# Optimization experiments

Measured on AMD Instinct MI355X. Metric: run time of the kernel, lower is better.

Reference implementation:

```python
import jax, jax.numpy as jnp
import numpy as np

S, B, H = 256, 64, 1024


def setup_inputs() -> dict:
    key = jax.random.key(0)
    ks = jax.random.split(key, 8)
    scale = 1.0 / np.sqrt(2 * H)  # nn.Linear default-ish scale
    return {
        "x": jax.random.normal(ks[0], (S, B, H), dtype=jnp.float32),
        "h0": jax.random.normal(ks[1], (B, H), dtype=jnp.float32),
        "c0": jax.random.normal(ks[2], (B, H), dtype=jnp.float32),
        "Wf": jax.random.normal(ks[3], (H, 2 * H), dtype=jnp.float32) * scale,
        "bf": jnp.zeros((H,), dtype=jnp.float32),
        "Wi": jax.random.normal(ks[4], (H, 2 * H), dtype=jnp.float32) * scale,
        "bi": jnp.zeros((H,), dtype=jnp.float32),
        "Wg": jax.random.normal(ks[5], (H, 2 * H), dtype=jnp.float32) * scale,
        "bg": jnp.zeros((H,), dtype=jnp.float32),
        "Wo": jax.random.normal(ks[6], (H, 2 * H), dtype=jnp.float32) * scale,
        "bo": jnp.zeros((H,), dtype=jnp.float32),
    }


def _lstm(x, h0, c0, Wf, bf, Wi, bi, Wg, bg, Wo, bo):
    nhid = h0.shape[-1]
    # Fuse the 4 gate Linears into one GEMM: W_all [4H, 2H], b_all [4H].
    W_all = jnp.concatenate([Wf, Wi, Wg, Wo], axis=0)
    b_all = jnp.concatenate([bf, bi, bg, bo], axis=0)
    Wx, Wh = W_all[:, :nhid], W_all[:, nhid:]  # x-part / h-part of cat([x,h])
    # Precompute input contribution for all timesteps: [S, B, 4H]
    xz = jnp.einsum("sbh,gh->sbg", x, Wx) + b_all

    def step(carry, xz_t):
        h, c = carry
        z = xz_t + h @ Wh.T  # [B, 4H]
        f, i, g, o = jnp.split(z, 4, axis=-1)
        f = jax.nn.sigmoid(f)
        i = jax.nn.sigmoid(i)
        g = jnp.tanh(g)
        o = jax.nn.sigmoid(o)
        c = f * c + i * g
        h = o * jnp.tanh(c)
        return (h, c), h

    (h_f, c_f), hseq = jax.lax.scan(step, (h0, c0), xz)
    return hseq, h_f, c_f


def reference(x, h0, c0, Wf, bf, Wi, bi, Wg, bg, Wo, bo):
    hseq, h_f, c_f = _lstm(x, h0, c0, Wf, bf, Wi, bi, Wg, bg, Wo, bo)
    # residual_con=False path in the original: return x + hidden_seq
    return x + hseq, h_f, c_f
```

## Files before the change

kernel.cpp:

```cpp
#include <hip/hip_runtime.h>

typedef __bf16 bf16x8 __attribute__((ext_vector_type(8)));
typedef float f32x4 __attribute__((ext_vector_type(4)));
typedef unsigned int u32x4 __attribute__((ext_vector_type(4)));

#define S_LEN 256
#define BATCH 64
#define HID   1024
#define NWG   256
#define SBH   (S_LEN * BATCH * HID)
#define BH    (BATCH * HID)
#define BAR_INTS 256

__device__ __forceinline__ float sigm(float v) { return 1.0f / (1.0f + __expf(-v)); }
__device__ __forceinline__ float tanh_fast(float v) {
  float e = __expf(-2.0f * __builtin_fabsf(v));
  float r = (1.0f - e) / (1.0f + e);
  return __builtin_copysignf(r, v);
}

__device__ __forceinline__ u32x4 cvt8(float4 a, float4 b) {
  union { unsigned short us[8]; u32x4 v; } r;
  r.us[0] = __builtin_bit_cast(unsigned short, (__bf16)a.x);
  r.us[1] = __builtin_bit_cast(unsigned short, (__bf16)a.y);
  r.us[2] = __builtin_bit_cast(unsigned short, (__bf16)a.z);
  r.us[3] = __builtin_bit_cast(unsigned short, (__bf16)a.w);
  r.us[4] = __builtin_bit_cast(unsigned short, (__bf16)b.x);
  r.us[5] = __builtin_bit_cast(unsigned short, (__bf16)b.y);
  r.us[6] = __builtin_bit_cast(unsigned short, (__bf16)b.z);
  r.us[7] = __builtin_bit_cast(unsigned short, (__bf16)b.w);
  return r.v;
}

#define LOAD8_X4(dst, base, MODS)                                             \
  asm volatile(                                                               \
      "global_load_dwordx4 %0, %8, off offset:0 " MODS "\n\t"                 \
      "global_load_dwordx4 %1, %8, off offset:64 " MODS "\n\t"                \
      "global_load_dwordx4 %2, %8, off offset:128 " MODS "\n\t"               \
      "global_load_dwordx4 %3, %8, off offset:192 " MODS "\n\t"               \
      "global_load_dwordx4 %4, %8, off offset:256 " MODS "\n\t"               \
      "global_load_dwordx4 %5, %8, off offset:320 " MODS "\n\t"               \
      "global_load_dwordx4 %6, %8, off offset:384 " MODS "\n\t"               \
      "global_load_dwordx4 %7, %8, off offset:448 " MODS "\n\t"               \
      "s_waitcnt vmcnt(0)"                                                    \
      : "=&v"((dst)[0]), "=&v"((dst)[1]), "=&v"((dst)[2]), "=&v"((dst)[3]),   \
        "=&v"((dst)[4]), "=&v"((dst)[5]), "=&v"((dst)[6]), "=&v"((dst)[7])    \
      : "v"(base)                                                             \
      : "memory")

__global__ void prep_kernel(const float* __restrict__ x, const float* __restrict__ h0,
                            const float* __restrict__ Wf, const float* __restrict__ Wi,
                            const float* __restrict__ Wg, const float* __restrict__ Wo,
                            __bf16* __restrict__ x_bf, __bf16* __restrict__ w_x,
                            __bf16* __restrict__ w_h, __bf16* __restrict__ h_buf,
                            int* __restrict__ bar) {
  size_t tid = (size_t)blockIdx.x * blockDim.x + threadIdx.x;
  size_t stride = (size_t)gridDim.x * blockDim.x;

  for (size_t i = tid; i < (size_t)(SBH / 8); i += stride) {
    const float4* s = (const float4*)x + i * 2;
    ((u32x4*)x_bf)[i] = cvt8(s[0], s[1]);
  }

#define W_CONV(W, gidx)                                                        \
  for (size_t i = tid; i < (size_t)(1024 * 128); i += stride) {                \
    int j   = (int)(i >> 7);                                                   \
    int kc8 = (int)(i & 127);                                                  \
    const float* row = (W) + (size_t)j * 2048;                                 \
    const float4* sx = (const float4*)(row + kc8 * 8);                         \
    const float4* sh = (const float4*)(row + 1024 + kc8 * 8);                  \
    size_t dst = (size_t)((gidx) * 1024 + j) * 128 + kc8;                      \
    ((u32x4*)w_x)[dst] = cvt8(sx[0], sx[1]);                                   \
    ((u32x4*)w_h)[dst] = cvt8(sh[0], sh[1]);                                   \
  }
  W_CONV(Wf, 0)
  W_CONV(Wi, 1)
  W_CONV(Wg, 2)
  W_CONV(Wo, 3)
#undef W_CONV

  for (size_t i = tid; i < (size_t)(BH / 8); i += stride) {
    const float4* s = (const float4*)h0 + i * 2;
    ((u32x4*)h_buf)[i] = cvt8(s[0], s[1]);
  }

  for (size_t i = tid; i < BAR_INTS; i += stride) bar[i] = 0;
}

__global__ __launch_bounds__(256, 1) void lstm_kernel(
    const float* __restrict__ x, const float* __restrict__ c0,
    const float* __restrict__ bfp, const float* __restrict__ bip,
    const float* __restrict__ bgp, const float* __restrict__ bop,
    const __bf16* __restrict__ x_bf, const __bf16* __restrict__ w_x,
    const __bf16* __restrict__ w_h, __bf16* __restrict__ h_buf,
    int* __restrict__ bar, float* __restrict__ out) {
  const int tid    = threadIdx.x;
  const int wgid   = blockIdx.x;
  const int m_idx  = wgid & 3;
  const int m_base = m_idx * 16;
  const int U      = (wgid >> 2) * 16;
  const int wave   = tid >> 6;
  const int lane   = tid & 63;
  const int l16    = lane & 15;
  const int kq8    = (lane >> 4) * 8;
  const int kbase  = wave * 256;
  const int wg_in_grp = wgid >> 2;

  int* slots = bar + m_idx * 64;

  __shared__ float zbuf[4][16][65];
  __shared__ __bf16 hpack[16][16];

  u32x4 Braw[64];
#pragma unroll
  for (int n = 0; n < 4; ++n) {
    unsigned long gbh =
        (unsigned long)(w_h + (size_t)(n * 1024 + U + l16) * HID + kbase + kq8);
    LOAD8_X4(&Braw[n * 8], gbh, "");
  }
#pragma unroll
  for (int n = 0; n < 4; ++n) {
    unsigned long gbx =
        (unsigned long)(w_x + (size_t)(n * 1024 + U + l16) * HID + kbase + kq8);
    LOAD8_X4(&Braw[32 + n * 8], gbx, "");
  }

  const int b_loc  = tid >> 4;
  const int u_loc  = tid & 15;
  const int j_t    = U + u_loc;
  const int b_glob = m_base + b_loc;
  float c = c0[(size_t)b_glob * HID + j_t];
  const float bias_f = bfp[j_t], bias_i = bip[j_t], bias_g = bgp[j_t], bias_o = bop[j_t];

  u32x4 Araw_x[8];
  {
    const __bf16* xp = x_bf + (size_t)(m_base + l16) * HID + kbase + kq8;
#pragma unroll
    for (int kc = 0; kc < 8; ++kc) Araw_x[kc] = *(const u32x4*)(xp + kc * 32);
  }
  f32x4 accx0 = {0,0,0,0}, accx1 = {0,0,0,0}, accx2 = {0,0,0,0}, accx3 = {0,0,0,0};
#pragma unroll
  for (int kc = 0; kc < 8; ++kc) {
    bf16x8 a = __builtin_bit_cast(bf16x8, Araw_x[kc]);
    accx0 = __builtin_amdgcn_mfma_f32_16x16x32_bf16(a, __builtin_bit_cast(bf16x8, Braw[32 +  0 + kc]), accx0, 0, 0, 0);
    accx1 = __builtin_amdgcn_mfma_f32_16x16x32_bf16(a, __builtin_bit_cast(bf16x8, Braw[32 +  8 + kc]), accx1, 0, 0, 0);
    accx2 = __builtin_amdgcn_mfma_f32_16x16x32_bf16(a, __builtin_bit_cast(bf16x8, Braw[32 + 16 + kc]), accx2, 0, 0, 0);
    accx3 = __builtin_amdgcn_mfma_f32_16x16x32_bf16(a, __builtin_bit_cast(bf16x8, Braw[32 + 24 + kc]), accx3, 0, 0, 0);
  }
  {
    const __bf16* xp = x_bf + (size_t)(BATCH + m_base + l16) * HID + kbase + kq8;
#pragma unroll
    for (int kc = 0; kc < 8; ++kc) Araw_x[kc] = *(const u32x4*)(xp + kc * 32);
  }

  for (int t = 0; t < S_LEN; ++t) {
    const size_t roff = (t & 1) ? (size_t)BH : 0;
    const size_t woff = (t & 1) ? 0 : (size_t)BH;

    u32x4 Araw_h[8];
    {
      unsigned long ga = (unsigned long)(h_buf + roff + (size_t)(m_base + l16) * HID +
                                         kbase + kq8);
      LOAD8_X4(Araw_h, ga, "sc0 sc1");
    }

    f32x4 acc0 = accx0, acc1 = accx1, acc2 = accx2, acc3 = accx3;
#pragma unroll
    for (int kc = 0; kc < 8; ++kc) {
      bf16x8 a = __builtin_bit_cast(bf16x8, Araw_h[kc]);
      acc0 = __builtin_amdgcn_mfma_f32_16x16x32_bf16(a, __builtin_bit_cast(bf16x8, Braw[ 0 + kc]), acc0, 0, 0, 0);
      acc1 = __builtin_amdgcn_mfma_f32_16x16x32_bf16(a, __builtin_bit_cast(bf16x8, Braw[ 8 + kc]), acc1, 0, 0, 0);
      acc2 = __builtin_amdgcn_mfma_f32_16x16x32_bf16(a, __builtin_bit_cast(bf16x8, Braw[16 + kc]), acc2, 0, 0, 0);
      acc3 = __builtin_amdgcn_mfma_f32_16x16x32_bf16(a, __builtin_bit_cast(bf16x8, Braw[24 + kc]), acc3, 0, 0, 0);
    }

    {
      int q = lane >> 4;
#pragma unroll
      for (int r = 0; r < 4; ++r) {
        zbuf[wave][q * 4 + r][ 0 + l16] = acc0[r];
        zbuf[wave][q * 4 + r][16 + l16] = acc1[r];
        zbuf[wave][q * 4 + r][32 + l16] = acc2[r];
        zbuf[wave][q * 4 + r][48 + l16] = acc3[r];
      }
    }
    __syncthreads();

    float h;
    {
      float zf = 0.f, zi = 0.f, zg = 0.f, zo = 0.f;
#pragma unroll
      for (int w = 0; w < 4; ++w) {
        zf += zbuf[w][b_loc][ 0 + u_loc];
        zi += zbuf[w][b_loc][16 + u_loc];
        zg += zbuf[w][b_loc][32 + u_loc];
        zo += zbuf[w][b_loc][48 + u_loc];
      }
      float fg = sigm(zf + bias_f);
      float ig = sigm(zi + bias_i);
      float gg = tanh_fast(zg + bias_g);
      float og = sigm(zo + bias_o);
      c = fg * c + ig * gg;
      h = og * tanh_fast(c);
    }

    if (t < S_LEN - 1) {
      hpack[b_loc][u_loc] = (__bf16)h;
      __syncthreads();

      if (tid < 32) {
        int b = tid >> 1, hf = tid & 1;
        u32x4 hv = *(const u32x4*)(&hpack[b][hf * 8]);
        unsigned long ha = (unsigned long)(h_buf + woff +
                                           (size_t)(m_base + b) * HID + U + hf * 8);
        asm volatile("global_store_dwordx4 %0, %1, off sc0 sc1\n\t"
                     "s_waitcnt vmcnt(0)"
                     :: "v"(ha), "v"(hv) : "memory");
      }
      if (tid == 0) {
        __hip_atomic_store(&slots[wg_in_grp], t + 1,
                           __ATOMIC_RELAXED, __HIP_MEMORY_SCOPE_AGENT);
      }

      {
        size_t oi = ((size_t)(t * BATCH + b_glob)) * HID + j_t;
        out[oi] = x[oi] + h;
      }
      accx0 = (f32x4){0,0,0,0}; accx1 = (f32x4){0,0,0,0};
      accx2 = (f32x4){0,0,0,0}; accx3 = (f32x4){0,0,0,0};
#pragma unroll
      for (int kc = 0; kc < 8; ++kc) {
        bf16x8 a = __builtin_bit_cast(bf16x8, Araw_x[kc]);
        accx0 = __builtin_amdgcn_mfma_f32_16x16x32_bf16(a, __builtin_bit_cast(bf16x8, Braw[32 +  0 + kc]), accx0, 0, 0, 0);
        accx1 = __builtin_amdgcn_mfma_f32_16x16x32_bf16(a, __builtin_bit_cast(bf16x8, Braw[32 +  8 + kc]), accx1, 0, 0, 0);
        accx2 = __builtin_amdgcn_mfma_f32_16x16x32_bf16(a, __builtin_bit_cast(bf16x8, Braw[32 + 16 + kc]), accx2, 0, 0, 0);
        accx3 = __builtin_amdgcn_mfma_f32_16x16x32_bf16(a, __builtin_bit_cast(bf16x8, Braw[32 + 24 + kc]), accx3, 0, 0, 0);
      }
      {
        int tn = (t + 2 < S_LEN) ? (t + 2) : (S_LEN - 1);
        const __bf16* xp =
            x_bf + ((size_t)(tn * BATCH + m_base + l16)) * HID + kbase + kq8;
#pragma unroll
        for (int kc = 0; kc < 8; ++kc) Araw_x[kc] = *(const u32x4*)(xp + kc * 32);
      }

      if (wave == 1) {
        const int target = t + 1;
        while (true) {
          int v = __hip_atomic_load(&slots[lane],
                                    __ATOMIC_RELAXED, __HIP_MEMORY_SCOPE_AGENT);
          if (__ballot(v >= target) == ~0ull) break;
          __builtin_amdgcn_s_sleep(1);
        }
      }
      __syncthreads();
    } else {
      size_t oi = ((size_t)(t * BATCH + b_glob)) * HID + j_t;
      out[oi] = x[oi] + h;
      out[(size_t)SBH + (size_t)b_glob * HID + j_t] = h;
      out[(size_t)SBH + BH + (size_t)b_glob * HID + j_t] = c;
    }
  }
}

extern "C" void kernel_launch(void* const* d_in, const int* in_sizes, int n_in,
                              void* d_out, int out_size, void* d_ws, size_t ws_size,
                              hipStream_t stream) {
  const float* x   = (const float*)d_in[0];
  const float* h0  = (const float*)d_in[1];
  const float* c0  = (const float*)d_in[2];
  const float* Wf  = (const float*)d_in[3];
  const float* bf_ = (const float*)d_in[4];
  const float* Wi  = (const float*)d_in[5];
  const float* bi_ = (const float*)d_in[6];
  const float* Wg  = (const float*)d_in[7];
  const float* bg_ = (const float*)d_in[8];
  const float* Wo  = (const float*)d_in[9];
  const float* bo_ = (const float*)d_in[10];

  char* ws = (char*)d_ws;
  size_t off = 0;
  __bf16* x_bf = (__bf16*)(ws + off); off += (size_t)SBH * 2;
  __bf16* w_x  = (__bf16*)(ws + off); off += (size_t)4 * 1024 * 1024 * 2;
  __bf16* w_h  = (__bf16*)(ws + off); off += (size_t)4 * 1024 * 1024 * 2;
  __bf16* h_buf = (__bf16*)(ws + off); off += (size_t)2 * BH * 2;
  int* bar = (int*)(ws + off); off += BAR_INTS * sizeof(int);
  if (ws_size < off) return;

  float* out = (float*)d_out;

  prep_kernel<<<2048, 256, 0, stream>>>(x, h0, Wf, Wi, Wg, Wo, x_bf, w_x, w_h, h_buf, bar);
  lstm_kernel<<<NWG, 256, 0, stream>>>(x, c0, bf_, bi_, bg_, bo_, x_bf, w_x, w_h, h_buf, bar, out);
}
```

Baseline: 1.207 ms.

## Replace atomic slot barrier with parity bits embedded in bf16 h data

Drops the per-step atomic flag barrier between workgroups. Instead, the lowest mantissa bit of every bf16 h value carries the timestep parity, and readers spin-reload h until all parity bits match the expected value. zbuf is double-buffered and a __syncthreads is dropped, so consecutive steps can overlap without a full block barrier. This removes the store-flag-then-poll round trip and the wait after the store. The cost is one bit of h precision and a reliance on 16-byte stores being seen atomically.

```diff
diff --git a/kernel.cpp b/kernel.cpp
--- a/kernel.cpp
+++ b/kernel.cpp
@@ -10,7 +10,6 @@
 #define NWG   256
 #define SBH   (S_LEN * BATCH * HID)
 #define BH    (BATCH * HID)
-#define BAR_INTS 256
 
 __device__ __forceinline__ float sigm(float v) { return 1.0f / (1.0f + __expf(-v)); }
 __device__ __forceinline__ float tanh_fast(float v) {
@@ -52,8 +51,7 @@
                             const float* __restrict__ Wf, const float* __restrict__ Wi,
                             const float* __restrict__ Wg, const float* __restrict__ Wo,
                             __bf16* __restrict__ x_bf, __bf16* __restrict__ w_x,
-                            __bf16* __restrict__ w_h, __bf16* __restrict__ h_buf,
-                            int* __restrict__ bar) {
+                            __bf16* __restrict__ w_h, __bf16* __restrict__ h_buf) {
   size_t tid = (size_t)blockIdx.x * blockDim.x + threadIdx.x;
   size_t stride = (size_t)gridDim.x * blockDim.x;
 
@@ -81,10 +79,15 @@
 
   for (size_t i = tid; i < (size_t)(BH / 8); i += stride) {
     const float4* s = (const float4*)h0 + i * 2;
-    ((u32x4*)h_buf)[i] = cvt8(s[0], s[1]);
-  }
-
-  for (size_t i = tid; i < BAR_INTS; i += stride) bar[i] = 0;
+    u32x4 v = cvt8(s[0], s[1]);
+    v &= 0xFFFEFFFEu;
+    ((u32x4*)h_buf)[i] = v;
+  }
+
+  for (size_t i = tid; i < (size_t)(BH / 8); i += stride) {
+    u32x4 p = {0x00010001u, 0x00010001u, 0x00010001u, 0x00010001u};
+    ((u32x4*)(h_buf + BH))[i] = p;
+  }
 }
 
 __global__ __launch_bounds__(256, 1) void lstm_kernel(
@@ -93,7 +96,7 @@
     const float* __restrict__ bgp, const float* __restrict__ bop,
     const __bf16* __restrict__ x_bf, const __bf16* __restrict__ w_x,
     const __bf16* __restrict__ w_h, __bf16* __restrict__ h_buf,
-    int* __restrict__ bar, float* __restrict__ out) {
+    float* __restrict__ out) {
   const int tid    = threadIdx.x;
   const int wgid   = blockIdx.x;
   const int m_idx  = wgid & 3;
@@ -104,12 +107,9 @@
   const int l16    = lane & 15;
   const int kq8    = (lane >> 4) * 8;
   const int kbase  = wave * 256;
-  const int wg_in_grp = wgid >> 2;
-
-  int* slots = bar + m_idx * 64;
-
-  __shared__ float zbuf[4][16][65];
-  __shared__ __bf16 hpack[16][16];
+
+  __shared__ float zbuf[2][4][16][65];
+  __shared__ unsigned short hpack[16][16];
 
   u32x4 Braw[64];
 #pragma unroll
@@ -156,12 +156,28 @@
   for (int t = 0; t < S_LEN; ++t) {
     const size_t roff = (t & 1) ? (size_t)BH : 0;
     const size_t woff = (t & 1) ? 0 : (size_t)BH;
+    const int zp = t & 1;
 
     u32x4 Araw_h[8];
     {
       unsigned long ga = (unsigned long)(h_buf + roff + (size_t)(m_base + l16) * HID +
                                          kbase + kq8);
+      const unsigned mexp = ((unsigned)(t >> 1) & 1u) * 0x00010001u;
       LOAD8_X4(Araw_h, ga, "sc0 sc1");
+      while (true) {
+        unsigned bad = 0;
+#pragma unroll
+        for (int kc = 0; kc < 8; ++kc) {
+          u32x4 w = Araw_h[kc];
+          bad |= ((w[0] ^ mexp) & 0x00010001u);
+          bad |= ((w[1] ^ mexp) & 0x00010001u);
+          bad |= ((w[2] ^ mexp) & 0x00010001u);
+          bad |= ((w[3] ^ mexp) & 0x00010001u);
+        }
+        if (__ballot(bad != 0) == 0ull) break;
+        __builtin_amdgcn_s_sleep(2);
+        LOAD8_X4(Araw_h, ga, "sc0 sc1");
+      }
     }
 
     f32x4 acc0 = accx0, acc1 = accx1, acc2 = accx2, acc3 = accx3;
@@ -178,10 +194,10 @@
       int q = lane >> 4;
 #pragma unroll
       for (int r = 0; r < 4; ++r) {
-        zbuf[wave][q * 4 + r][ 0 + l16] = acc0[r];
-        zbuf[wave][q * 4 + r][16 + l16] = acc1[r];
-        zbuf[wave][q * 4 + r][32 + l16] = acc2[r];
-        zbuf[wave][q * 4 + r][48 + l16] = acc3[r];
+        zbuf[zp][wave][q * 4 + r][ 0 + l16] = acc0[r];
+        zbuf[zp][wave][q * 4 + r][16 + l16] = acc1[r];
+        zbuf[zp][wave][q * 4 + r][32 + l16] = acc2[r];
+        zbuf[zp][wave][q * 4 + r][48 + l16] = acc3[r];
       }
     }
     __syncthreads();
@@ -191,10 +207,10 @@
       float zf = 0.f, zi = 0.f, zg = 0.f, zo = 0.f;
 #pragma unroll
       for (int w = 0; w < 4; ++w) {
-        zf += zbuf[w][b_loc][ 0 + u_loc];
-        zi += zbuf[w][b_loc][16 + u_loc];
-        zg += zbuf[w][b_loc][32 + u_loc];
-        zo += zbuf[w][b_loc][48 + u_loc];
+        zf += zbuf[zp][w][b_loc][ 0 + u_loc];
+        zi += zbuf[zp][w][b_loc][16 + u_loc];
+        zg += zbuf[zp][w][b_loc][32 + u_loc];
+        zo += zbuf[zp][w][b_loc][48 + u_loc];
       }
       float fg = sigm(zf + bias_f);
       float ig = sigm(zi + bias_i);
@@ -205,21 +221,20 @@
     }
 
     if (t < S_LEN - 1) {
-      hpack[b_loc][u_loc] = (__bf16)h;
-      __syncthreads();
-
-      if (tid < 32) {
-        int b = tid >> 1, hf = tid & 1;
-        u32x4 hv = *(const u32x4*)(&hpack[b][hf * 8]);
+      {
+        unsigned short hb = __builtin_bit_cast(unsigned short, (__bf16)h);
+        hb = (unsigned short)((hb & 0xFFFEu) | (unsigned)(((t + 1) >> 1) & 1));
+        hpack[b_loc][u_loc] = hb;
+      }
+      asm volatile("s_waitcnt lgkmcnt(0)" ::: "memory");
+      __builtin_amdgcn_sched_barrier(0);
+      if (lane < 8) {
+        int b = 4 * wave + (lane >> 1), half = lane & 1;
+        u32x4 hv = *(const u32x4*)(&hpack[b][half * 8]);
         unsigned long ha = (unsigned long)(h_buf + woff +
-                                           (size_t)(m_base + b) * HID + U + hf * 8);
-        asm volatile("global_store_dwordx4 %0, %1, off sc0 sc1\n\t"
-                     "s_waitcnt vmcnt(0)"
+                                           (size_t)(m_base + b) * HID + U + half * 8);
+        asm volatile("global_store_dwordx4 %0, %1, off sc0 sc1"
                      :: "v"(ha), "v"(hv) : "memory");
-      }
-      if (tid == 0) {
-        __hip_atomic_store(&slots[wg_in_grp], t + 1,
-                           __ATOMIC_RELAXED, __HIP_MEMORY_SCOPE_AGENT);
       }
 
       {
@@ -243,17 +258,6 @@
 #pragma unroll
         for (int kc = 0; kc < 8; ++kc) Araw_x[kc] = *(const u32x4*)(xp + kc * 32);
       }
-
-      if (wave == 1) {
-        const int target = t + 1;
-        while (true) {
-          int v = __hip_atomic_load(&slots[lane],
-                                    __ATOMIC_RELAXED, __HIP_MEMORY_SCOPE_AGENT);
-          if (__ballot(v >= target) == ~0ull) break;
-          __builtin_amdgcn_s_sleep(1);
-        }
-      }
-      __syncthreads();
     } else {
       size_t oi = ((size_t)(t * BATCH + b_glob)) * HID + j_t;
       out[oi] = x[oi] + h;
@@ -284,11 +288,10 @@
   __bf16* w_x  = (__bf16*)(ws + off); off += (size_t)4 * 1024 * 1024 * 2;
   __bf16* w_h  = (__bf16*)(ws + off); off += (size_t)4 * 1024 * 1024 * 2;
   __bf16* h_buf = (__bf16*)(ws + off); off += (size_t)2 * BH * 2;
-  int* bar = (int*)(ws + off); off += BAR_INTS * sizeof(int);
   if (ws_size < off) return;
 
   float* out = (float*)d_out;
 
-  prep_kernel<<<2048, 256, 0, stream>>>(x, h0, Wf, Wi, Wg, Wo, x_bf, w_x, w_h, h_buf, bar);
-  lstm_kernel<<<NWG, 256, 0, stream>>>(x, c0, bf_, bi_, bg_, bo_, x_bf, w_x, w_h, h_buf, bar, out);
-}
+  prep_kernel<<<2048, 256, 0, stream>>>(x, h0, Wf, Wi, Wg, Wo, x_bf, w_x, w_h, h_buf);
+  lstm_kernel<<<NWG, 256, 0, stream>>>(x, c0, bf_, bi_, bg_, bo_, x_bf, w_x, w_h, h_buf, out);
+}
```

Measured after the change: 1.071 ms. -11.3%, faster.
